# Performance work log

Measured on AMD Instinct MI355X. Metric: run time of the kernel, lower is better.

The kernel has to match this reference:

```python
import jax, jax.numpy as jnp
import numpy as np

D_MODEL, D_K, D_V = 1024, 64, 64

def setup_inputs() -> dict:
    key = jax.random.key(0)
    ks = jax.random.split(key, 9)
    B, S = 8, 2048
    scale = 1.0 / np.sqrt(D_MODEL)
    return {
        "q_input": jax.random.normal(ks[0], (B, S, D_MODEL), jnp.float32),
        "k_input": jax.random.normal(ks[1], (B, S, D_MODEL), jnp.float32),
        "v_input": jax.random.normal(ks[2], (B, S, D_MODEL), jnp.float32),
        "Wq": jax.random.normal(ks[3], (D_K, D_MODEL), jnp.float32) * scale,
        "bq": jnp.zeros((D_K,), jnp.float32),
        "Wk": jax.random.normal(ks[4], (D_K, D_MODEL), jnp.float32) * scale,
        "bk": jnp.zeros((D_K,), jnp.float32),
        "Wv": jax.random.normal(ks[5], (D_V, D_MODEL), jnp.float32) * scale,
        "bv": jnp.zeros((D_V,), jnp.float32),
    }

def reference(q_input, k_input, v_input, Wq, bq, Wk, bk, Wv, bv):
    # Linear projections (torch Linear: x @ W^T + b)
    q = jnp.einsum('bsm,km->bsk', q_input, Wq) + bq  # [B,S,d_k]
    k = jnp.einsum('bsm,km->bsk', k_input, Wk) + bk  # [B,S,d_k]
    v = jnp.einsum('bsm,vm->bsv', v_input, Wv) + bv  # [B,S,d_v]
    scores = jnp.einsum('bqk,bsk->bqs', q, k) / jnp.sqrt(jnp.float32(D_K))
    # source applies causal mask unconditionally (is_mask is never None)
    S = q_input.shape[1]
    causal = jnp.tril(jnp.ones((S, S), bool))
    scores = jnp.where(causal[None], scores, jnp.float32(-1e9))
    attn = jax.nn.softmax(scores, axis=2)
    return jnp.einsum('bqs,bsv->bqv', attn, v)
```

## Files before the change

kernel.cpp:

```cpp
#include <hip/hip_runtime.h>
#include <hip/hip_bf16.h>

#define B_ 8
#define S_ 2048
#define DM 1024
#define DK 64

typedef __attribute__((ext_vector_type(8))) short bf16x8;
typedef __attribute__((ext_vector_type(4))) float f32x4;
typedef __attribute__((ext_vector_type(4))) short short4_t;
typedef unsigned int u32;

__device__ __forceinline__ short bf16s(float f) {
    union { float f; unsigned u; } v; v.f = f;
    unsigned r = v.u + 0x7fffu + ((v.u >> 16) & 1u);
    return (short)(r >> 16);
}

__device__ __forceinline__ void gl_lds16(const void* g, void* l) {
    __builtin_amdgcn_global_load_lds(
        (const __attribute__((address_space(1))) u32*)g,
        (__attribute__((address_space(3))) u32*)l, 16, 0, 0);
}

__global__ __launch_bounds__(256) void convw_kernel(
    const float* __restrict__ Wq, const float* __restrict__ Wk,
    const float* __restrict__ Wv, short* __restrict__ wbf)
{
    const int i = (blockIdx.x * 256 + threadIdx.x) * 8;
    const float* src = (i < 65536) ? Wq : (i < 131072) ? Wk : Wv;
    const int off = i & 65535;
    float4 f0 = *(const float4*)(src + off);
    float4 f1 = *(const float4*)(src + off + 4);
    bf16x8 o;
    o[0]=bf16s(f0.x); o[1]=bf16s(f0.y); o[2]=bf16s(f0.z); o[3]=bf16s(f0.w);
    o[4]=bf16s(f1.x); o[5]=bf16s(f1.y); o[6]=bf16s(f1.z); o[7]=bf16s(f1.w);
    *(bf16x8*)(wbf + i) = o;
}

__global__ __launch_bounds__(256) void proj_kernel(
    const float* __restrict__ xq, const float* __restrict__ xk, const float* __restrict__ xv,
    const short* __restrict__ wbf,
    const float* __restrict__ bq, const float* __restrict__ bk, const float* __restrict__ bv,
    short* __restrict__ q_ws, short* __restrict__ k_ws, short* __restrict__ vt_ws)
{
    __shared__ __align__(16) char smem[49152];

    const int which = blockIdx.y;
    const float* x    = (which == 0) ? xq : (which == 1) ? xk : xv;
    const float* bias = (which == 0) ? bq : (which == 1) ? bk : bv;
    const short* wsrc = wbf + which * (DK * DM);

    const int tid = threadIdx.x;
    const int w   = tid >> 6;
    const int i   = tid & 63;
    const int lr  = i & 15;
    const int g   = i >> 4;
    const int row0 = blockIdx.x * 64;

    const int rot = (blockIdx.x * 5 + which * 7) & 15;

    f32x4 acc[4];
    #pragma unroll
    for (int f = 0; f < 4; ++f) acc[f] = f32x4{0.f, 0.f, 0.f, 0.f};

    auto stage = [&](int buf, int kc) {
        char* xd = smem + buf * 16384 + (w * 16) * 256;
        const float* xrow = x + (long)(row0 + w * 16) * DM + kc;
        #pragma unroll
        for (int j = 0; j < 4; ++j) {
            const int rl  = j * 4 + (i >> 4);
            const int byt = ((i & 15) * 16) ^ ((rl & 7) << 5);
            gl_lds16((const char*)(xrow + (long)rl * DM) + byt, xd + j * 1024);
        }
        char* wd = smem + 32768 + buf * 8192 + (w * 16) * 128;
        const short* wrow = wsrc + (long)(w * 16) * DM + kc;
        #pragma unroll
        for (int j = 0; j < 2; ++j) {
            const int nl  = j * 8 + (i >> 3);
            const int byt = ((i & 7) * 16) ^ ((nl & 7) << 4);
            gl_lds16((const char*)(wrow + (long)nl * DM) + byt, wd + j * 1024);
        }
    };

    auto compute = [&](int buf) {
        const char* xr = smem + buf * 16384 + (w * 16 + lr) * 256;
        const char* wr = smem + 32768 + buf * 8192;
        const int sx = (lr & 7) << 5;
        const int sw = (lr & 7) << 4;
        #pragma unroll
        for (int ks = 0; ks < 2; ++ks) {
            const int bA = (ks * 128 + g * 32) ^ sx;
            f32x4 x0 = *(const f32x4*)(xr + bA);
            f32x4 x1 = *(const f32x4*)(xr + bA + 16);
            bf16x8 af;
            af[0]=bf16s(x0[0]); af[1]=bf16s(x0[1]); af[2]=bf16s(x0[2]); af[3]=bf16s(x0[3]);
            af[4]=bf16s(x1[0]); af[5]=bf16s(x1[1]); af[6]=bf16s(x1[2]); af[7]=bf16s(x1[3]);
            const int bB = (ks * 64 + g * 16) ^ sw;
            #pragma unroll
            for (int f = 0; f < 4; ++f) {
                bf16x8 wf = *(const bf16x8*)(wr + (f * 16 + lr) * 128 + bB);
                acc[f] = __builtin_amdgcn_mfma_f32_16x16x32_bf16(af, wf, acc[f], 0, 0, 0);
            }
        }
    };

    stage(0, rot * 64);
    __builtin_amdgcn_sched_barrier(0);
    stage(1, ((1 + rot) & 15) * 64);
    __builtin_amdgcn_sched_barrier(0);

    #pragma unroll 2
    for (int t = 0; t < 16; ++t) {
        if (t < 15) asm volatile("s_waitcnt vmcnt(6)" ::: "memory");
        else        asm volatile("s_waitcnt vmcnt(0)" ::: "memory");
        asm volatile("s_barrier" ::: "memory");
        const int buf = t & 1;
        compute(buf);
        asm volatile("s_waitcnt lgkmcnt(0)" ::: "memory");
        asm volatile("s_barrier" ::: "memory");
        if (t + 2 < 16) stage(buf, ((t + 2 + rot) & 15) * 64);
    }

    if (which < 2) {
        short* stile = (short*)smem + w * 1024;
        #pragma unroll
        for (int f = 0; f < 4; ++f) {
            float bb = bias[f * 16 + lr];
            #pragma unroll
            for (int r = 0; r < 4; ++r)
                stile[(g * 4 + r) * 64 + f * 16 + lr] = bf16s(acc[f][r] + bb);
        }
        asm volatile("s_waitcnt lgkmcnt(0)" ::: "memory");
        __builtin_amdgcn_sched_barrier(0);
        short* outp = (which == 0) ? q_ws : k_ws;
        const long gbase = (long)(row0 + w * 16) * 64;
        *(bf16x8*)(outp + gbase +       i * 8) = *(const bf16x8*)(&stile[i * 8]);
        *(bf16x8*)(outp + gbase + 512 + i * 8) = *(const bf16x8*)(&stile[512 + i * 8]);
    } else {
        const int rw = row0 + w * 16;
        const int b = rw >> 11;
        const int s = (rw & 2047) + g * 4;
        #pragma unroll
        for (int f = 0; f < 4; ++f) {
            float bb = bias[f * 16 + lr];
            short4_t st;
            st[0]=bf16s(acc[f][0]+bb); st[1]=bf16s(acc[f][1]+bb);
            st[2]=bf16s(acc[f][2]+bb); st[3]=bf16s(acc[f][3]+bb);
            *(short4_t*)(vt_ws + (long)(b * 64 + f * 16 + lr) * S_ + s) = st;
        }
    }
}

__global__ __launch_bounds__(256) void attn_kernel(
    const short* __restrict__ q_ws, const short* __restrict__ k_ws,
    const short* __restrict__ vt_ws, float* __restrict__ out)
{
    __shared__ __align__(16) short plds[4][16 * 40];
    __shared__ __align__(16) float accds[4][64][16];
    __shared__ __align__(16) float2 mlds[4][16];

    const int n = blockIdx.x;
    const int c = n & 255, s = n >> 8;
    const int u = c & 127, v = c >> 7;
    const int b  = v * 4 + s;
    const int qt = (s & 1) ? (127 - u) : u;
    const int qbase = qt * 16;
    const int kend  = qbase + 16;
    const int niter = (kend + 31) >> 5;

    const int tid  = threadIdx.x;
    const int wv   = tid >> 6;
    const int lane = tid & 63;
    const int lr = lane & 15, g = lane >> 4, lk = g * 8;
    const int q_glob = qbase + lr;

    const short* qp = q_ws + ((long)b * S_ + qbase + lr) * DK;
    const bf16x8 qb0 = *(const bf16x8*)(qp + lk);
    const bf16x8 qb1 = *(const bf16x8*)(qp + 32 + lk);
    const short* kb = k_ws  + (long)b * S_ * DK;
    const short* vb = vt_ws + (long)b * DK * S_;

    float m = -INFINITY, l = 0.f;
    f32x4 acc[4];
    #pragma unroll
    for (int f = 0; f < 4; ++f) acc[f] = f32x4{0.f, 0.f, 0.f, 0.f};
    const float sc = 0.125f * 1.44269504088896340736f;

    short* pw = plds[wv];
    for (int t = wv; t < niter; t += 4) {
        const int kv = t * 32;
        const bool sub1 = (kv + 16) < kend;
        bf16x8 vf0 = *(const bf16x8*)(vb + (long)(lr)      * S_ + kv + lk);
        bf16x8 vf1 = *(const bf16x8*)(vb + (long)(16 + lr) * S_ + kv + lk);
        bf16x8 vf2 = *(const bf16x8*)(vb + (long)(32 + lr) * S_ + kv + lk);
        bf16x8 vf3 = *(const bf16x8*)(vb + (long)(48 + lr) * S_ + kv + lk);

        const short* kp0 = kb + (long)(kv + lr) * DK;
        bf16x8 k00 = *(const bf16x8*)(kp0 + lk);
        bf16x8 k01 = *(const bf16x8*)(kp0 + 32 + lk);
        f32x4 s0 = f32x4{0.f,0.f,0.f,0.f};
        s0 = __builtin_amdgcn_mfma_f32_16x16x32_bf16(k00, qb0, s0, 0, 0, 0);
        s0 = __builtin_amdgcn_mfma_f32_16x16x32_bf16(k01, qb1, s0, 0, 0, 0);
        f32x4 s1 = f32x4{0.f,0.f,0.f,0.f};
        if (sub1) {
            const short* kp1 = kp0 + 16 * DK;
            bf16x8 k10 = *(const bf16x8*)(kp1 + lk);
            bf16x8 k11 = *(const bf16x8*)(kp1 + 32 + lk);
            s1 = __builtin_amdgcn_mfma_f32_16x16x32_bf16(k10, qb0, s1, 0, 0, 0);
            s1 = __builtin_amdgcn_mfma_f32_16x16x32_bf16(k11, qb1, s1, 0, 0, 0);
        }

        float pv[8];
        #pragma unroll
        for (int r = 0; r < 4; ++r) {
            const int key0 = kv + g*4 + r;
            pv[r]     = (key0 <= q_glob) ? s0[r] * sc : -INFINITY;
            const int key1 = kv + 16 + g*4 + r;
            pv[4 + r] = (sub1 && key1 <= q_glob) ? s1[r] * sc : -INFINITY;
        }
        float tm = fmaxf(fmaxf(fmaxf(pv[0],pv[1]), fmaxf(pv[2],pv[3])),
                         fmaxf(fmaxf(pv[4],pv[5]), fmaxf(pv[6],pv[7])));
        tm = fmaxf(tm, __shfl_xor(tm, 16));
        tm = fmaxf(tm, __shfl_xor(tm, 32));
        const float mn  = fmaxf(m, tm);
        const float fac = exp2f(m - mn);
        float ps = 0.f;
        #pragma unroll
        for (int q = 0; q < 8; ++q) { pv[q] = exp2f(pv[q] - mn); ps += pv[q]; }
        ps += __shfl_xor(ps, 16);
        ps += __shfl_xor(ps, 32);
        l = l * fac + ps;
        m = mn;
        #pragma unroll
        for (int f = 0; f < 4; ++f)
            #pragma unroll
            for (int r = 0; r < 4; ++r) acc[f][r] *= fac;

        short4_t pw0, pw1;
        pw0[0]=bf16s(pv[0]); pw0[1]=bf16s(pv[1]); pw0[2]=bf16s(pv[2]); pw0[3]=bf16s(pv[3]);
        pw1[0]=bf16s(pv[4]); pw1[1]=bf16s(pv[5]); pw1[2]=bf16s(pv[6]); pw1[3]=bf16s(pv[7]);
        *(short4_t*)(pw + lr*40 + g*4)      = pw0;
        *(short4_t*)(pw + lr*40 + 16 + g*4) = pw1;
        asm volatile("s_waitcnt lgkmcnt(0)" ::: "memory");
        __builtin_amdgcn_sched_barrier(0);
        const bf16x8 pf = *(const bf16x8*)(pw + lr*40 + lk);

        acc[0] = __builtin_amdgcn_mfma_f32_16x16x32_bf16(vf0, pf, acc[0], 0, 0, 0);
        acc[1] = __builtin_amdgcn_mfma_f32_16x16x32_bf16(vf1, pf, acc[1], 0, 0, 0);
        acc[2] = __builtin_amdgcn_mfma_f32_16x16x32_bf16(vf2, pf, acc[2], 0, 0, 0);
        acc[3] = __builtin_amdgcn_mfma_f32_16x16x32_bf16(vf3, pf, acc[3], 0, 0, 0);
    }

    #pragma unroll
    for (int f = 0; f < 4; ++f)
        *(f32x4*)(&accds[wv][lane][f * 4]) = acc[f];
    if (g == 0) mlds[wv][lr] = float2{m, l};
    __syncthreads();

    const float2 ml0 = mlds[0][lr], ml1 = mlds[1][lr],
                 ml2 = mlds[2][lr], ml3 = mlds[3][lr];
    const float M = fmaxf(fmaxf(ml0.x, ml1.x), fmaxf(ml2.x, ml3.x));
    const float w0 = exp2f(ml0.x - M), w1 = exp2f(ml1.x - M),
                w2 = exp2f(ml2.x - M), w3 = exp2f(ml3.x - M);
    const float L = w0*ml0.y + w1*ml1.y + w2*ml2.y + w3*ml3.y;
    f32x4 o = w0 * (*(const f32x4*)(&accds[0][lane][wv * 4]))
            + w1 * (*(const f32x4*)(&accds[1][lane][wv * 4]))
            + w2 * (*(const f32x4*)(&accds[2][lane][wv * 4]))
            + w3 * (*(const f32x4*)(&accds[3][lane][wv * 4]));
    const float inv = 1.0f / L;
    o[0]*=inv; o[1]*=inv; o[2]*=inv; o[3]*=inv;
    *(f32x4*)(out + ((long)b * S_ + qbase + lr) * DK + wv * 16 + g * 4) = o;
}

extern "C" void kernel_launch(void* const* d_in, const int* in_sizes, int n_in,
                              void* d_out, int out_size, void* d_ws, size_t ws_size,
                              hipStream_t stream) {
    const float* q_in = (const float*)d_in[0];
    const float* k_in = (const float*)d_in[1];
    const float* v_in = (const float*)d_in[2];
    const float* Wq   = (const float*)d_in[3];
    const float* bq   = (const float*)d_in[4];
    const float* Wk   = (const float*)d_in[5];
    const float* bk   = (const float*)d_in[6];
    const float* Wv   = (const float*)d_in[7];
    const float* bv   = (const float*)d_in[8];

    short* q_ws  = (short*)d_ws;
    short* k_ws  = q_ws + (size_t)B_ * S_ * DK;
    short* vt_ws = k_ws + (size_t)B_ * S_ * DK;
    short* wbf   = vt_ws + (size_t)B_ * S_ * DK;
    float* out   = (float*)d_out;

    convw_kernel<<<dim3(96), 256, 0, stream>>>(Wq, Wk, Wv, wbf);
    proj_kernel<<<dim3((B_ * S_) / 64, 3), 256, 0, stream>>>(
        q_in, k_in, v_in, wbf, bq, bk, bv, q_ws, k_ws, vt_ws);
    attn_kernel<<<dim3(B_ * 128), 256, 0, stream>>>(q_ws, k_ws, vt_ws, out);
}
```

Measured before the change: 74.18 us.

## Stage projection tiles through registers instead of direct global-to-LDS loads

Replaces the global_load_lds direct-to-shared loads in the projection kernel with ordinary vector global loads into registers, followed by explicit swizzled LDS stores. The main loop becomes a manually unrolled ping-pong: the next chunk's loads are issued while computing on the current shared-memory buffer, and the waits rely on the compiler instead of hand-tuned vmcnt waits. The aim is better overlap and control of load latency against MFMA work. The cost is extra VGPRs and extra LDS write instructions per chunk.

```diff
diff --git a/kernel.cpp b/kernel.cpp
--- a/kernel.cpp
+++ b/kernel.cpp
@@ -15,12 +15,6 @@
     union { float f; unsigned u; } v; v.f = f;
     unsigned r = v.u + 0x7fffu + ((v.u >> 16) & 1u);
     return (short)(r >> 16);
-}
-
-__device__ __forceinline__ void gl_lds16(const void* g, void* l) {
-    __builtin_amdgcn_global_load_lds(
-        (const __attribute__((address_space(1))) u32*)g,
-        (__attribute__((address_space(3))) u32*)l, 16, 0, 0);
 }
 
 __global__ __launch_bounds__(256) void convw_kernel(
@@ -64,22 +58,32 @@
     #pragma unroll
     for (int f = 0; f < 4; ++f) acc[f] = f32x4{0.f, 0.f, 0.f, 0.f};
 
-    auto stage = [&](int buf, int kc) {
+    auto fetch = [&](f32x4 (&xb)[4], f32x4 (&wb)[2], int kc) {
+        const float* xrow = x + (long)(row0 + w * 16) * DM + kc;
+        #pragma unroll
+        for (int j = 0; j < 4; ++j) {
+            const int rl = j * 4 + g;
+            xb[j] = *(const f32x4*)((const char*)(xrow + (long)rl * DM) + (i & 15) * 16);
+        }
+        const short* wrow = wsrc + (long)(w * 16) * DM + kc;
+        #pragma unroll
+        for (int j = 0; j < 2; ++j) {
+            const int nl = j * 8 + (i >> 3);
+            wb[j] = *(const f32x4*)((const char*)(wrow + (long)nl * DM) + (i & 7) * 16);
+        }
+    };
+    auto writeLDS = [&](const f32x4 (&xb)[4], const f32x4 (&wb)[2], int buf) {
         char* xd = smem + buf * 16384 + (w * 16) * 256;
-        const float* xrow = x + (long)(row0 + w * 16) * DM + kc;
         #pragma unroll
         for (int j = 0; j < 4; ++j) {
-            const int rl  = j * 4 + (i >> 4);
-            const int byt = ((i & 15) * 16) ^ ((rl & 7) << 5);
-            gl_lds16((const char*)(xrow + (long)rl * DM) + byt, xd + j * 1024);
+            const int rl = j * 4 + g;
+            *(f32x4*)(xd + rl * 256 + (((i & 15) * 16) ^ ((rl & 7) << 5))) = xb[j];
         }
         char* wd = smem + 32768 + buf * 8192 + (w * 16) * 128;
-        const short* wrow = wsrc + (long)(w * 16) * DM + kc;
         #pragma unroll
         for (int j = 0; j < 2; ++j) {
-            const int nl  = j * 8 + (i >> 3);
-            const int byt = ((i & 7) * 16) ^ ((nl & 7) << 4);
-            gl_lds16((const char*)(wrow + (long)nl * DM) + byt, wd + j * 1024);
+            const int nl = j * 8 + (i >> 3);
+            *(f32x4*)(wd + nl * 128 + (((i & 7) * 16) ^ ((nl & 7) << 4))) = wb[j];
         }
     };
 
@@ -105,21 +109,26 @@
         }
     };
 
-    stage(0, rot * 64);
-    __builtin_amdgcn_sched_barrier(0);
-    stage(1, ((1 + rot) & 15) * 64);
-    __builtin_amdgcn_sched_barrier(0);
-
-    #pragma unroll 2
-    for (int t = 0; t < 16; ++t) {
-        if (t < 15) asm volatile("s_waitcnt vmcnt(6)" ::: "memory");
-        else        asm volatile("s_waitcnt vmcnt(0)" ::: "memory");
-        asm volatile("s_barrier" ::: "memory");
-        const int buf = t & 1;
-        compute(buf);
+    f32x4 xA[4], wA[2], xB[4], wB[2];
+    fetch(xA, wA, rot * 64);
+    writeLDS(xA, wA, 0);
+    fetch(xB, wB, ((1 + rot) & 15) * 64);
+    asm volatile("s_waitcnt lgkmcnt(0)" ::: "memory");
+    asm volatile("s_barrier" ::: "memory");
+
+    for (int t = 0; t < 16; t += 2) {
+        compute(0);
+        if (t + 2 < 16) fetch(xA, wA, ((t + 2 + rot) & 15) * 64);
+        writeLDS(xB, wB, 1);
         asm volatile("s_waitcnt lgkmcnt(0)" ::: "memory");
         asm volatile("s_barrier" ::: "memory");
-        if (t + 2 < 16) stage(buf, ((t + 2 + rot) & 15) * 64);
+        compute(1);
+        if (t + 3 < 16) fetch(xB, wB, ((t + 3 + rot) & 15) * 64);
+        if (t + 2 < 16) {
+            writeLDS(xA, wA, 0);
+            asm volatile("s_waitcnt lgkmcnt(0)" ::: "memory");
+        }
+        asm volatile("s_barrier" ::: "memory");
     }
 
     if (which < 2) {
```

Result: no change. 75.01 us (+1.1%).
